# Kernel optimization log

Measured on AMD Instinct MI355X. Metric: run time of the kernel, lower is better.

The kernel has to match this reference:

```python
import jax, jax.numpy as jnp
import numpy as np

N = 50000   # nodes
E = 640000  # edges
IN_C, HID_C, OUT_C = 128, 128, 64


def _glorot(key, shape):
    lim = float(np.sqrt(6.0 / (shape[0] + shape[1])))
    return jax.random.uniform(key, shape, jnp.float32, -lim, lim)


def setup_inputs() -> dict:
    key = jax.random.key(0)
    ks = jax.random.split(key, 6)
    x = jax.random.normal(ks[0], (N, IN_C), jnp.float32)
    edge_index = jax.random.randint(ks[1], (2, E), 0, N, dtype=jnp.int64)
    W1 = _glorot(ks[2], (IN_C, HID_C));  b1 = jnp.zeros((HID_C,), jnp.float32)
    W2 = _glorot(ks[3], (HID_C, HID_C)); b2 = jnp.zeros((HID_C,), jnp.float32)
    W3 = _glorot(ks[4], (HID_C, OUT_C)); b3 = jnp.zeros((OUT_C,), jnp.float32)
    return {"x": x, "edge_index": edge_index,
            "W1": W1, "b1": b1, "W2": W2, "b2": b2, "W3": W3, "b3": b3}


def gcn_conv(x, W, b, src, dst, n_nodes):
    """PyG GCNConv (eval): add self-loops, D^-1/2 (A+I) D^-1/2, linear, bias."""
    h = x @ W  # [N, out]
    ones = jnp.ones(src.shape[0], h.dtype)
    # degree including the self-loop (+1 per node)
    deg = jax.ops.segment_sum(ones, dst, num_segments=n_nodes) + 1.0
    dinv_sqrt = jax.lax.rsqrt(deg)
    coef = dinv_sqrt[src] * dinv_sqrt[dst]               # [E]
    agg = jax.ops.segment_sum(h[src] * coef[:, None], dst, num_segments=n_nodes)
    agg = agg + h * (1.0 / deg)[:, None]                 # self-loop term: 1/deg[i]
    return agg + b


def reference(x, edge_index, W1, b1, W2, b2, W3, b3):
    src, dst = edge_index[0], edge_index[1]
    h = jax.nn.relu(gcn_conv(x, W1, b1, src, dst, N))
    h = jax.nn.relu(gcn_conv(h, W2, b2, src, dst, N))
    return gcn_conv(h, W3, b3, src, dst, N)
```

## Files before the change

kernel.cpp:

```cpp
#include <hip/hip_runtime.h>


#define K_DIM 128

typedef __attribute__((ext_vector_type(8))) short bf16x8;
typedef __attribute__((ext_vector_type(4))) float f32x4;

__device__ __forceinline__ unsigned short f2bf(float x) {
    unsigned u = __float_as_uint(x);
    return (unsigned short)((u + 0x7fffu + ((u >> 16) & 1u)) >> 16);
}
__device__ __forceinline__ float bflo(unsigned v) { return __uint_as_float(v << 16); }
__device__ __forceinline__ float bfhi(unsigned v) { return __uint_as_float(v & 0xffff0000u); }


__global__ void k_zero_int(int* __restrict__ p, int n) {
    int i = blockIdx.x * 256 + threadIdx.x;
    if (i < n) p[i] = 0;
}

__global__ void k_count(const int* __restrict__ dst, int* __restrict__ cnt, int E) {
    int e = blockIdx.x * 256 + threadIdx.x;
    if (e < E) atomicAdd(&cnt[dst[e]], 1);
}

__global__ void k_scan_block(const int* __restrict__ cnt, int* __restrict__ rowptr,
                             int* __restrict__ bsum, float* __restrict__ rsd, int n) {
    __shared__ int s[256];
    int t = threadIdx.x;
    int i = blockIdx.x * 256 + t;
    int x = (i < n) ? cnt[i] : 0;
    if (i < n) rsd[i] = rsqrtf((float)x + 1.0f);
    s[t] = x;
    __syncthreads();
#pragma unroll
    for (int d = 1; d < 256; d <<= 1) {
        int v = (t >= d) ? s[t - d] : 0;
        __syncthreads();
        s[t] += v;
        __syncthreads();
    }
    if (i < n) rowptr[i] = s[t] - x;
    if (t == 255) bsum[blockIdx.x] = s[255];
}

__global__ void k_scan_bsums(int* __restrict__ bsum, int nb) {
    __shared__ int s[256];
    int t = threadIdx.x;
    int x = (t < nb) ? bsum[t] : 0;
    s[t] = x;
    __syncthreads();
#pragma unroll
    for (int d = 1; d < 256; d <<= 1) {
        int v = (t >= d) ? s[t - d] : 0;
        __syncthreads();
        s[t] += v;
        __syncthreads();
    }
    if (t < nb) bsum[t] = s[t] - x;
}

__global__ void k_scan_add(int* __restrict__ rowptr, int* __restrict__ cursor,
                           const int* __restrict__ bsum, int n, int E) {
    int i = blockIdx.x * 256 + threadIdx.x;
    if (i < n) {
        int v = rowptr[i] + bsum[i >> 8];
        rowptr[i] = v;
        cursor[i] = v;
    }
    if (i == 0) rowptr[n] = E;
}

__global__ void k_fill(const int* __restrict__ src, const int* __restrict__ dst,
                       int* __restrict__ cursor, int* __restrict__ col, int E) {
    int e = blockIdx.x * 256 + threadIdx.x;
    if (e < E) {
        int d = dst[e];
        int pos = atomicAdd(&cursor[d], 1);
        col[pos] = src[e];
    }
}

__global__ void k_cvt(const float* __restrict__ x, unsigned short* __restrict__ Xb,
                      const float* __restrict__ W1, const float* __restrict__ W2,
                      const float* __restrict__ W3,
                      unsigned short* __restrict__ Wt1, unsigned short* __restrict__ Wt2,
                      unsigned short* __restrict__ Wt3, int nx4) {
    int i = blockIdx.x * 256 + threadIdx.x;
    if (i < nx4) {
        float4 v = *(const float4*)&x[(size_t)i * 4];
        ushort4 o;
        o.x = f2bf(v.x); o.y = f2bf(v.y); o.z = f2bf(v.z); o.w = f2bf(v.w);
        *(ushort4*)&Xb[(size_t)i * 4] = o;
        return;
    }
    int j = i - nx4;
    if (j < 16384) { int n = j >> 7, k = j & 127; Wt1[n * 128 + k] = f2bf(W1[k * 128 + n]); return; }
    j -= 16384;
    if (j < 16384) { int n = j >> 7, k = j & 127; Wt2[n * 128 + k] = f2bf(W2[k * 128 + n]); return; }
    j -= 16384;
    if (j < 8192)  { int n = j >> 7, k = j & 127; Wt3[n * 128 + k] = f2bf(W3[k * 64 + n]); return; }
}

template <int COUT>
__launch_bounds__(256)
__global__ void k_gemm_mfma(const unsigned short* __restrict__ A,
                            const unsigned short* __restrict__ Wt,
                            const float* __restrict__ rsd,
                            unsigned short* __restrict__ Hb, int nrows) {
    constexpr int NT = COUT / 16;
    const int wave = threadIdx.x >> 6;
    const int lane = threadIdx.x & 63;
    const int m16 = lane & 15;
    const int kg  = lane >> 4;
    const int r0w = blockIdx.x * 64 + wave * 16;

    int arow = r0w + m16;
    if (arow >= nrows) arow = nrows - 1;

    bf16x8 a[4];
#pragma unroll
    for (int kb = 0; kb < 4; ++kb)
        a[kb] = *(const bf16x8*)&A[(size_t)arow * 128 + kb * 32 + kg * 8];

    f32x4 acc[NT];
#pragma unroll
    for (int t = 0; t < NT; ++t) acc[t] = (f32x4){0.f, 0.f, 0.f, 0.f};

#pragma unroll
    for (int t = 0; t < NT; ++t) {
        const unsigned short* wp = &Wt[(size_t)(t * 16 + m16) * 128 + kg * 8];
#pragma unroll
        for (int kb = 0; kb < 4; ++kb) {
            bf16x8 b = *(const bf16x8*)&wp[kb * 32];
            acc[t] = __builtin_amdgcn_mfma_f32_16x16x32_bf16(a[kb], b, acc[t], 0, 0, 0);
        }
    }

    const int rowb = r0w + kg * 4;
    float rs[4];
#pragma unroll
    for (int i = 0; i < 4; ++i)
        rs[i] = (rowb + i < nrows) ? rsd[rowb + i] : 0.0f;

#pragma unroll
    for (int t = 0; t < NT; ++t) {
#pragma unroll
        for (int i = 0; i < 4; ++i) {
            int r = rowb + i;
            if (r < nrows)
                Hb[(size_t)r * COUT + t * 16 + m16] = f2bf(acc[t][i] * rs[i]);
        }
    }
}

template <int C>
__launch_bounds__(256)
__global__ void k_agg_bf(const unsigned short* __restrict__ Hb,
                         const int* __restrict__ rowptr, const int* __restrict__ col,
                         const float* __restrict__ rsd, const float* __restrict__ bias,
                         unsigned short* __restrict__ Ab, int n) {
    constexpr int TPN = C / 8;
    constexpr int NPB = 256 / TPN;
    const int node = blockIdx.x * NPB + threadIdx.x / TPN;
    const int c = (threadIdx.x % TPN) * 8;
    if (node >= n) return;

    float acc[8];
    {
        uint4 v = *(const uint4*)&Hb[(size_t)node * C + c];
        acc[0] = bflo(v.x); acc[1] = bfhi(v.x);
        acc[2] = bflo(v.y); acc[3] = bfhi(v.y);
        acc[4] = bflo(v.z); acc[5] = bfhi(v.z);
        acc[6] = bflo(v.w); acc[7] = bfhi(v.w);
    }
    int e = rowptr[node], end = rowptr[node + 1];
    for (; e + 1 < end; e += 2) {
        int s0 = col[e], s1 = col[e + 1];
        uint4 v0 = *(const uint4*)&Hb[(size_t)s0 * C + c];
        uint4 v1 = *(const uint4*)&Hb[(size_t)s1 * C + c];
        acc[0] += bflo(v0.x); acc[1] += bfhi(v0.x);
        acc[2] += bflo(v0.y); acc[3] += bfhi(v0.y);
        acc[4] += bflo(v0.z); acc[5] += bfhi(v0.z);
        acc[6] += bflo(v0.w); acc[7] += bfhi(v0.w);
        acc[0] += bflo(v1.x); acc[1] += bfhi(v1.x);
        acc[2] += bflo(v1.y); acc[3] += bfhi(v1.y);
        acc[4] += bflo(v1.z); acc[5] += bfhi(v1.z);
        acc[6] += bflo(v1.w); acc[7] += bfhi(v1.w);
    }
    if (e < end) {
        int s0 = col[e];
        uint4 v0 = *(const uint4*)&Hb[(size_t)s0 * C + c];
        acc[0] += bflo(v0.x); acc[1] += bfhi(v0.x);
        acc[2] += bflo(v0.y); acc[3] += bfhi(v0.y);
        acc[4] += bflo(v0.z); acc[5] += bfhi(v0.z);
        acc[6] += bflo(v0.w); acc[7] += bfhi(v0.w);
    }

    const float rs = rsd[node];
    const float4 b0 = *(const float4*)&bias[c];
    const float4 b1 = *(const float4*)&bias[c + 4];
    float r[8];
    r[0] = fmaxf(b0.x + rs * acc[0], 0.0f); r[1] = fmaxf(b0.y + rs * acc[1], 0.0f);
    r[2] = fmaxf(b0.z + rs * acc[2], 0.0f); r[3] = fmaxf(b0.w + rs * acc[3], 0.0f);
    r[4] = fmaxf(b1.x + rs * acc[4], 0.0f); r[5] = fmaxf(b1.y + rs * acc[5], 0.0f);
    r[6] = fmaxf(b1.z + rs * acc[6], 0.0f); r[7] = fmaxf(b1.w + rs * acc[7], 0.0f);

    uint4 o;
    o.x = (unsigned)f2bf(r[0]) | ((unsigned)f2bf(r[1]) << 16);
    o.y = (unsigned)f2bf(r[2]) | ((unsigned)f2bf(r[3]) << 16);
    o.z = (unsigned)f2bf(r[4]) | ((unsigned)f2bf(r[5]) << 16);
    o.w = (unsigned)f2bf(r[6]) | ((unsigned)f2bf(r[7]) << 16);
    *(uint4*)&Ab[(size_t)node * C + c] = o;
}

template <int C>
__launch_bounds__(256)
__global__ void k_agg_final(const unsigned short* __restrict__ Hb,
                            const int* __restrict__ rowptr, const int* __restrict__ col,
                            const float* __restrict__ rsd, const float* __restrict__ bias,
                            float* __restrict__ OUT, int n) {
    constexpr int TPN = C / 8;
    constexpr int NPB = 256 / TPN;
    const int node = blockIdx.x * NPB + threadIdx.x / TPN;
    const int c = (threadIdx.x % TPN) * 8;
    if (node >= n) return;

    float acc[8];
    {
        uint4 v = *(const uint4*)&Hb[(size_t)node * C + c];
        acc[0] = bflo(v.x); acc[1] = bfhi(v.x);
        acc[2] = bflo(v.y); acc[3] = bfhi(v.y);
        acc[4] = bflo(v.z); acc[5] = bfhi(v.z);
        acc[6] = bflo(v.w); acc[7] = bfhi(v.w);
    }
    int e = rowptr[node], end = rowptr[node + 1];
    for (; e + 1 < end; e += 2) {
        int s0 = col[e], s1 = col[e + 1];
        uint4 v0 = *(const uint4*)&Hb[(size_t)s0 * C + c];
        uint4 v1 = *(const uint4*)&Hb[(size_t)s1 * C + c];
        acc[0] += bflo(v0.x); acc[1] += bfhi(v0.x);
        acc[2] += bflo(v0.y); acc[3] += bfhi(v0.y);
        acc[4] += bflo(v0.z); acc[5] += bfhi(v0.z);
        acc[6] += bflo(v0.w); acc[7] += bfhi(v0.w);
        acc[0] += bflo(v1.x); acc[1] += bfhi(v1.x);
        acc[2] += bflo(v1.y); acc[3] += bfhi(v1.y);
        acc[4] += bflo(v1.z); acc[5] += bfhi(v1.z);
        acc[6] += bflo(v1.w); acc[7] += bfhi(v1.w);
    }
    if (e < end) {
        int s0 = col[e];
        uint4 v0 = *(const uint4*)&Hb[(size_t)s0 * C + c];
        acc[0] += bflo(v0.x); acc[1] += bfhi(v0.x);
        acc[2] += bflo(v0.y); acc[3] += bfhi(v0.y);
        acc[4] += bflo(v0.z); acc[5] += bfhi(v0.z);
        acc[6] += bflo(v0.w); acc[7] += bfhi(v0.w);
    }

    const float rs = rsd[node];
    const float4 b0 = *(const float4*)&bias[c];
    const float4 b1 = *(const float4*)&bias[c + 4];
    float* po = &OUT[(size_t)node * C + c];
    *(float4*)&po[0] = make_float4(b0.x + rs * acc[0], b0.y + rs * acc[1],
                                   b0.z + rs * acc[2], b0.w + rs * acc[3]);
    *(float4*)&po[4] = make_float4(b1.x + rs * acc[4], b1.y + rs * acc[5],
                                   b1.z + rs * acc[6], b1.w + rs * acc[7]);
}


extern "C" void kernel_launch(void* const* d_in, const int* in_sizes, int n_in,
                              void* d_out, int out_size, void* d_ws, size_t ws_size,
                              hipStream_t stream) {
    const float* x  = (const float*)d_in[0];
    const int*   ei = (const int*)d_in[1];
    const float* W1 = (const float*)d_in[2];
    const float* b1 = (const float*)d_in[3];
    const float* W2 = (const float*)d_in[4];
    const float* b2 = (const float*)d_in[5];
    const float* W3 = (const float*)d_in[6];
    const float* b3 = (const float*)d_in[7];

    const int N = in_sizes[0] / K_DIM;
    const int E = in_sizes[1] / 2;
    const int* srcv = ei;
    const int* dstv = ei + E;

    char* ws = (char*)d_ws;
    size_t off = 0;
    auto alloc = [&](size_t bytes) {
        char* p = ws + off;
        off += (bytes + 255) & ~(size_t)255;
        return p;
    };
    int*   cnt    = (int*)alloc((size_t)N * 4);
    int*   rowptr = (int*)alloc((size_t)(N + 1) * 4);
    int*   cursor = (int*)alloc((size_t)N * 4);
    int*   bsum   = (int*)alloc(256 * 4);
    float* rsd    = (float*)alloc((size_t)N * 4);
    int*   col    = (int*)alloc((size_t)E * 4);
    unsigned short* Xb  = (unsigned short*)alloc((size_t)N * 128 * 2);
    unsigned short* Wt1 = (unsigned short*)alloc(128 * 128 * 2);
    unsigned short* Wt2 = (unsigned short*)alloc(128 * 128 * 2);
    unsigned short* Wt3 = (unsigned short*)alloc(64 * 128 * 2);
    unsigned short* Hb1 = (unsigned short*)alloc((size_t)N * 128 * 2);
    unsigned short* Ab  = (unsigned short*)alloc((size_t)N * 128 * 2);
    unsigned short* Hb2 = (unsigned short*)alloc((size_t)N * 128 * 2);
    unsigned short* Hb3 = (unsigned short*)alloc((size_t)N * 64 * 2);
    float* out = (float*)d_out;

    const int gN = (N + 255) / 256;
    const int gE = (E + 255) / 256;
    const int gb = (N + 63) / 64;
    const int nb = gN;
    const int gA128 = (N + 15) / 16;
    const int gAF   = (N + 31) / 32;
    const int nx4   = N * 32;
    const int gCVT  = (nx4 + 16384 + 16384 + 8192 + 255) / 256;

    k_zero_int<<<gN, 256, 0, stream>>>(cnt, N);
    k_count<<<gE, 256, 0, stream>>>(dstv, cnt, E);
    k_scan_block<<<nb, 256, 0, stream>>>(cnt, rowptr, bsum, rsd, N);
    k_scan_bsums<<<1, 256, 0, stream>>>(bsum, nb);
    k_scan_add<<<gN, 256, 0, stream>>>(rowptr, cursor, bsum, N, E);
    k_fill<<<gE, 256, 0, stream>>>(srcv, dstv, cursor, col, E);

    k_cvt<<<gCVT, 256, 0, stream>>>(x, Xb, W1, W2, W3, Wt1, Wt2, Wt3, nx4);

    k_gemm_mfma<128><<<gb, 256, 0, stream>>>(Xb, Wt1, rsd, Hb1, N);
    k_agg_bf<128><<<gA128, 256, 0, stream>>>(Hb1, rowptr, col, rsd, b1, Ab, N);

    k_gemm_mfma<128><<<gb, 256, 0, stream>>>(Ab, Wt2, rsd, Hb2, N);
    k_agg_bf<128><<<gA128, 256, 0, stream>>>(Hb2, rowptr, col, rsd, b2, Ab, N);

    k_gemm_mfma<64><<<gb, 256, 0, stream>>>(Ab, Wt3, rsd, Hb3, N);
    k_agg_final<64><<<gAF, 256, 0, stream>>>(Hb3, rowptr, col, rsd, b3, out, N);
}
```

Baseline: 288.5 us.

## Fuse CSR build, input conversion and first GEMM into persistent megakernel

```diff
diff --git a/kernel.cpp b/kernel.cpp
--- a/kernel.cpp
+++ b/kernel.cpp
@@ -13,93 +13,164 @@
 __device__ __forceinline__ float bflo(unsigned v) { return __uint_as_float(v << 16); }
 __device__ __forceinline__ float bfhi(unsigned v) { return __uint_as_float(v & 0xffff0000u); }
 
-
-__global__ void k_zero_int(int* __restrict__ p, int n) {
-    int i = blockIdx.x * 256 + threadIdx.x;
-    if (i < n) p[i] = 0;
-}
-
-__global__ void k_count(const int* __restrict__ dst, int* __restrict__ cnt, int E) {
-    int e = blockIdx.x * 256 + threadIdx.x;
-    if (e < E) atomicAdd(&cnt[dst[e]], 1);
-}
-
-__global__ void k_scan_block(const int* __restrict__ cnt, int* __restrict__ rowptr,
-                             int* __restrict__ bsum, float* __restrict__ rsd, int n) {
+__device__ __forceinline__ void gbar(int* bar, int nb, int ph) {
+    __threadfence();
+    __syncthreads();
+    if (threadIdx.x == 0) {
+        atomicAdd(bar, 1);
+        while (atomicAdd(bar, 0) < nb * ph) __builtin_amdgcn_s_sleep(2);
+    }
+    __syncthreads();
+}
+
+template <int COUT>
+__device__ __forceinline__ void gemm_tile(const unsigned short* __restrict__ A,
+                                          const unsigned short* __restrict__ Wt,
+                                          const float* __restrict__ rsd,
+                                          unsigned short* __restrict__ Hb,
+                                          int nrows, int tile, int tid) {
+    constexpr int NT = COUT / 16;
+    const int wave = tid >> 6;
+    const int lane = tid & 63;
+    const int m16 = lane & 15;
+    const int kg  = lane >> 4;
+    const int r0w = tile * 64 + wave * 16;
+
+    int arow = r0w + m16;
+    if (arow >= nrows) arow = nrows - 1;
+
+    bf16x8 a[4];
+#pragma unroll
+    for (int kb = 0; kb < 4; ++kb)
+        a[kb] = *(const bf16x8*)&A[(size_t)arow * 128 + kb * 32 + kg * 8];
+
+    f32x4 acc[NT];
+#pragma unroll
+    for (int t = 0; t < NT; ++t) acc[t] = (f32x4){0.f, 0.f, 0.f, 0.f};
+
+#pragma unroll
+    for (int t = 0; t < NT; ++t) {
+        const unsigned short* wp = &Wt[(size_t)(t * 16 + m16) * 128 + kg * 8];
+#pragma unroll
+        for (int kb = 0; kb < 4; ++kb) {
+            bf16x8 b = *(const bf16x8*)&wp[kb * 32];
+            acc[t] = __builtin_amdgcn_mfma_f32_16x16x32_bf16(a[kb], b, acc[t], 0, 0, 0);
+        }
+    }
+
+    const int rowb = r0w + kg * 4;
+    float rs[4];
+#pragma unroll
+    for (int i = 0; i < 4; ++i)
+        rs[i] = (rowb + i < nrows) ? rsd[rowb + i] : 0.0f;
+
+#pragma unroll
+    for (int t = 0; t < NT; ++t) {
+#pragma unroll
+        for (int i = 0; i < 4; ++i) {
+            int r = rowb + i;
+            if (r < nrows)
+                Hb[(size_t)r * COUT + t * 16 + m16] = f2bf(acc[t][i] * rs[i]);
+        }
+    }
+}
+
+__global__ void k_init(int* __restrict__ cnt, int* __restrict__ bar,
+                       const float* __restrict__ W1, const float* __restrict__ W2,
+                       const float* __restrict__ W3,
+                       unsigned short* __restrict__ Wt1, unsigned short* __restrict__ Wt2,
+                       unsigned short* __restrict__ Wt3, int n) {
+    int g = blockIdx.x * 256 + threadIdx.x;
+    if (g < n) cnt[g] = 0;
+    if (g == 0) *bar = 0;
+    int j = g;
+    if (j < 16384) { int nn = j >> 7, k = j & 127; Wt1[nn * 128 + k] = f2bf(W1[k * 128 + nn]); return; }
+    j -= 16384;
+    if (j < 16384) { int nn = j >> 7, k = j & 127; Wt2[nn * 128 + k] = f2bf(W2[k * 128 + nn]); return; }
+    j -= 16384;
+    if (j < 8192)  { int nn = j >> 7, k = j & 127; Wt3[nn * 128 + k] = f2bf(W3[k * 64 + nn]); return; }
+}
+
+__global__ __launch_bounds__(256, 2)
+void k_mega(const float* __restrict__ x, const int* __restrict__ src,
+            const int* __restrict__ dst, int* __restrict__ cnt,
+            int* __restrict__ rowptr, int* __restrict__ cursor,
+            int* __restrict__ bsum, int* __restrict__ bsc,
+            float* __restrict__ rsd, int* __restrict__ col,
+            unsigned short* __restrict__ Xb, const unsigned short* __restrict__ Wt1,
+            unsigned short* __restrict__ Hb1, int* __restrict__ bar,
+            int N, int E, int nscan) {
+    const int nb = gridDim.x;
+    const int bid = blockIdx.x, tid = threadIdx.x;
+    const int gsz = nb * 256;
+    const int g = bid * 256 + tid;
     __shared__ int s[256];
-    int t = threadIdx.x;
-    int i = blockIdx.x * 256 + t;
-    int x = (i < n) ? cnt[i] : 0;
-    if (i < n) rsd[i] = rsqrtf((float)x + 1.0f);
-    s[t] = x;
-    __syncthreads();
-#pragma unroll
-    for (int d = 1; d < 256; d <<= 1) {
-        int v = (t >= d) ? s[t - d] : 0;
-        __syncthreads();
-        s[t] += v;
-        __syncthreads();
-    }
-    if (i < n) rowptr[i] = s[t] - x;
-    if (t == 255) bsum[blockIdx.x] = s[255];
-}
-
-__global__ void k_scan_bsums(int* __restrict__ bsum, int nb) {
-    __shared__ int s[256];
-    int t = threadIdx.x;
-    int x = (t < nb) ? bsum[t] : 0;
-    s[t] = x;
-    __syncthreads();
-#pragma unroll
-    for (int d = 1; d < 256; d <<= 1) {
-        int v = (t >= d) ? s[t - d] : 0;
-        __syncthreads();
-        s[t] += v;
-        __syncthreads();
-    }
-    if (t < nb) bsum[t] = s[t] - x;
-}
-
-__global__ void k_scan_add(int* __restrict__ rowptr, int* __restrict__ cursor,
-                           const int* __restrict__ bsum, int n, int E) {
-    int i = blockIdx.x * 256 + threadIdx.x;
-    if (i < n) {
-        int v = rowptr[i] + bsum[i >> 8];
-        rowptr[i] = v;
-        cursor[i] = v;
-    }
-    if (i == 0) rowptr[n] = E;
-}
-
-__global__ void k_fill(const int* __restrict__ src, const int* __restrict__ dst,
-                       int* __restrict__ cursor, int* __restrict__ col, int E) {
-    int e = blockIdx.x * 256 + threadIdx.x;
-    if (e < E) {
-        int d = dst[e];
-        int pos = atomicAdd(&cursor[d], 1);
-        col[pos] = src[e];
-    }
-}
-
-__global__ void k_cvt(const float* __restrict__ x, unsigned short* __restrict__ Xb,
-                      const float* __restrict__ W1, const float* __restrict__ W2,
-                      const float* __restrict__ W3,
-                      unsigned short* __restrict__ Wt1, unsigned short* __restrict__ Wt2,
-                      unsigned short* __restrict__ Wt3, int nx4) {
-    int i = blockIdx.x * 256 + threadIdx.x;
-    if (i < nx4) {
+
+    for (int e = g; e < E; e += gsz) atomicAdd(&cnt[dst[e]], 1);
+    const int nx4 = N * 32;
+    for (int i = g; i < nx4; i += gsz) {
         float4 v = *(const float4*)&x[(size_t)i * 4];
         ushort4 o;
         o.x = f2bf(v.x); o.y = f2bf(v.y); o.z = f2bf(v.z); o.w = f2bf(v.w);
         *(ushort4*)&Xb[(size_t)i * 4] = o;
-        return;
-    }
-    int j = i - nx4;
-    if (j < 16384) { int n = j >> 7, k = j & 127; Wt1[n * 128 + k] = f2bf(W1[k * 128 + n]); return; }
-    j -= 16384;
-    if (j < 16384) { int n = j >> 7, k = j & 127; Wt2[n * 128 + k] = f2bf(W2[k * 128 + n]); return; }
-    j -= 16384;
-    if (j < 8192)  { int n = j >> 7, k = j & 127; Wt3[n * 128 + k] = f2bf(W3[k * 64 + n]); return; }
+    }
+    gbar(bar, nb, 1);
+
+    if (bid < nscan) {
+        int i = bid * 256 + tid;
+        int v = (i < N) ? cnt[i] : 0;
+        if (i < N) rsd[i] = rsqrtf((float)v + 1.0f);
+        s[tid] = v;
+        __syncthreads();
+#pragma unroll
+        for (int d = 1; d < 256; d <<= 1) {
+            int u = (tid >= d) ? s[tid - d] : 0;
+            __syncthreads();
+            s[tid] += u;
+            __syncthreads();
+        }
+        if (i < N) rowptr[i] = s[tid] - v;
+        if (tid == 255) atomicExch(&bsum[bid], s[255]);
+    }
+    gbar(bar, nb, 2);
+
+    if (bid == 0) {
+        int v = (tid < nscan) ? atomicAdd(&bsum[tid], 0) : 0;
+        s[tid] = v;
+        __syncthreads();
+#pragma unroll
+        for (int d = 1; d < 256; d <<= 1) {
+            int u = (tid >= d) ? s[tid - d] : 0;
+            __syncthreads();
+            s[tid] += u;
+            __syncthreads();
+        }
+        if (tid < nscan) bsc[tid] = s[tid] - v;
+    }
+    gbar(bar, nb, 3);
+
+    if (bid < nscan) {
+        int off0 = bsc[bid];
+        int i = bid * 256 + tid;
+        if (i < N) {
+            int v = rowptr[i] + off0;
+            rowptr[i] = v;
+            cursor[i] = v;
+        }
+    }
+    if (g == 0) rowptr[N] = E;
+    gbar(bar, nb, 4);
+
+    for (int e = g; e < E; e += gsz) {
+        int d = dst[e];
+        int pos = atomicAdd(&cursor[d], 1);
+        col[pos] = src[e];
+    }
+    gbar(bar, nb, 5);
+
+    const int ntiles = (N + 63) >> 6;
+    for (int t = bid; t < ntiles; t += nb)
+        gemm_tile<128>(Xb, Wt1, rsd, Hb1, N, t, tid);
 }
 
 template <int COUT>
@@ -108,50 +179,7 @@
                             const unsigned short* __restrict__ Wt,
                             const float* __restrict__ rsd,
                             unsigned short* __restrict__ Hb, int nrows) {
-    constexpr int NT = COUT / 16;
-    const int wave = threadIdx.x >> 6;
-    const int lane = threadIdx.x & 63;
-    const int m16 = lane & 15;
-    const int kg  = lane >> 4;
-    const int r0w = blockIdx.x * 64 + wave * 16;
-
-    int arow = r0w + m16;
-    if (arow >= nrows) arow = nrows - 1;
-
-    bf16x8 a[4];
-#pragma unroll
-    for (int kb = 0; kb < 4; ++kb)
-        a[kb] = *(const bf16x8*)&A[(size_t)arow * 128 + kb * 32 + kg * 8];
-
-    f32x4 acc[NT];
-#pragma unroll
-    for (int t = 0; t < NT; ++t) acc[t] = (f32x4){0.f, 0.f, 0.f, 0.f};
-
-#pragma unroll
-    for (int t = 0; t < NT; ++t) {
-        const unsigned short* wp = &Wt[(size_t)(t * 16 + m16) * 128 + kg * 8];
-#pragma unroll
-        for (int kb = 0; kb < 4; ++kb) {
-            bf16x8 b = *(const bf16x8*)&wp[kb * 32];
-            acc[t] = __builtin_amdgcn_mfma_f32_16x16x32_bf16(a[kb], b, acc[t], 0, 0, 0);
-        }
-    }
-
-    const int rowb = r0w + kg * 4;
-    float rs[4];
-#pragma unroll
-    for (int i = 0; i < 4; ++i)
-        rs[i] = (rowb + i < nrows) ? rsd[rowb + i] : 0.0f;
-
-#pragma unroll
-    for (int t = 0; t < NT; ++t) {
-#pragma unroll
-        for (int i = 0; i < 4; ++i) {
-            int r = rowb + i;
-            if (r < nrows)
-                Hb[(size_t)r * COUT + t * 16 + m16] = f2bf(acc[t][i] * rs[i]);
-        }
-    }
+    gemm_tile<COUT>(A, Wt, rsd, Hb, nrows, blockIdx.x, threadIdx.x);
 }
 
 template <int C>
@@ -175,10 +203,12 @@
         acc[6] = bflo(v.w); acc[7] = bfhi(v.w);
     }
     int e = rowptr[node], end = rowptr[node + 1];
-    for (; e + 1 < end; e += 2) {
-        int s0 = col[e], s1 = col[e + 1];
+    for (; e + 3 < end; e += 4) {
+        int s0 = col[e], s1 = col[e + 1], s2 = col[e + 2], s3 = col[e + 3];
         uint4 v0 = *(const uint4*)&Hb[(size_t)s0 * C + c];
         uint4 v1 = *(const uint4*)&Hb[(size_t)s1 * C + c];
+        uint4 v2 = *(const uint4*)&Hb[(size_t)s2 * C + c];
+        uint4 v3 = *(const uint4*)&Hb[(size_t)s3 * C + c];
         acc[0] += bflo(v0.x); acc[1] += bfhi(v0.x);
         acc[2] += bflo(v0.y); acc[3] += bfhi(v0.y);
         acc[4] += bflo(v0.z); acc[5] += bfhi(v0.z);
@@ -187,8 +217,16 @@
         acc[2] += bflo(v1.y); acc[3] += bfhi(v1.y);
         acc[4] += bflo(v1.z); acc[5] += bfhi(v1.z);
         acc[6] += bflo(v1.w); acc[7] += bfhi(v1.w);
-    }
-    if (e < end) {
+        acc[0] += bflo(v2.x); acc[1] += bfhi(v2.x);
+        acc[2] += bflo(v2.y); acc[3] += bfhi(v2.y);
+        acc[4] += bflo(v2.z); acc[5] += bfhi(v2.z);
+        acc[6] += bflo(v2.w); acc[7] += bfhi(v2.w);
+        acc[0] += bflo(v3.x); acc[1] += bfhi(v3.x);
+        acc[2] += bflo(v3.y); acc[3] += bfhi(v3.y);
+        acc[4] += bflo(v3.z); acc[5] += bfhi(v3.z);
+        acc[6] += bflo(v3.w); acc[7] += bfhi(v3.w);
+    }
+    for (; e < end; ++e) {
         int s0 = col[e];
         uint4 v0 = *(const uint4*)&Hb[(size_t)s0 * C + c];
         acc[0] += bflo(v0.x); acc[1] += bfhi(v0.x);
@@ -235,10 +273,12 @@
         acc[6] = bflo(v.w); acc[7] = bfhi(v.w);
     }
     int e = rowptr[node], end = rowptr[node + 1];
-    for (; e + 1 < end; e += 2) {
-        int s0 = col[e], s1 = col[e + 1];
+    for (; e + 3 < end; e += 4) {
+        int s0 = col[e], s1 = col[e + 1], s2 = col[e + 2], s3 = col[e + 3];
         uint4 v0 = *(const uint4*)&Hb[(size_t)s0 * C + c];
         uint4 v1 = *(const uint4*)&Hb[(size_t)s1 * C + c];
+        uint4 v2 = *(const uint4*)&Hb[(size_t)s2 * C + c];
+        uint4 v3 = *(const uint4*)&Hb[(size_t)s3 * C + c];
         acc[0] += bflo(v0.x); acc[1] += bfhi(v0.x);
         acc[2] += bflo(v0.y); acc[3] += bfhi(v0.y);
         acc[4] += bflo(v0.z); acc[5] += bfhi(v0.z);
@@ -247,8 +287,16 @@
         acc[2] += bflo(v1.y); acc[3] += bfhi(v1.y);
         acc[4] += bflo(v1.z); acc[5] += bfhi(v1.z);
         acc[6] += bflo(v1.w); acc[7] += bfhi(v1.w);
-    }
-    if (e < end) {
+        acc[0] += bflo(v2.x); acc[1] += bfhi(v2.x);
+        acc[2] += bflo(v2.y); acc[3] += bfhi(v2.y);
+        acc[4] += bflo(v2.z); acc[5] += bfhi(v2.z);
+        acc[6] += bflo(v2.w); acc[7] += bfhi(v2.w);
+        acc[0] += bflo(v3.x); acc[1] += bfhi(v3.x);
+        acc[2] += bflo(v3.y); acc[3] += bfhi(v3.y);
+        acc[4] += bflo(v3.z); acc[5] += bfhi(v3.z);
+        acc[6] += bflo(v3.w); acc[7] += bfhi(v3.w);
+    }
+    for (; e < end; ++e) {
         int s0 = col[e];
         uint4 v0 = *(const uint4*)&Hb[(size_t)s0 * C + c];
         acc[0] += bflo(v0.x); acc[1] += bfhi(v0.x);
@@ -296,6 +344,8 @@
     int*   rowptr = (int*)alloc((size_t)(N + 1) * 4);
     int*   cursor = (int*)alloc((size_t)N * 4);
     int*   bsum   = (int*)alloc(256 * 4);
+    int*   bsc    = (int*)alloc(256 * 4);
+    int*   bar    = (int*)alloc(256);
     float* rsd    = (float*)alloc((size_t)N * 4);
     int*   col    = (int*)alloc((size_t)E * 4);
     unsigned short* Xb  = (unsigned short*)alloc((size_t)N * 128 * 2);
@@ -308,30 +358,20 @@
     unsigned short* Hb3 = (unsigned short*)alloc((size_t)N * 64 * 2);
     float* out = (float*)d_out;
 
-    const int gN = (N + 255) / 256;
-    const int gE = (E + 255) / 256;
-    const int gb = (N + 63) / 64;
-    const int nb = gN;
+    const int gN    = (N + 255) / 256;
+    const int gb    = (N + 63) / 64;
     const int gA128 = (N + 15) / 16;
     const int gAF   = (N + 31) / 32;
-    const int nx4   = N * 32;
-    const int gCVT  = (nx4 + 16384 + 16384 + 8192 + 255) / 256;
-
-    k_zero_int<<<gN, 256, 0, stream>>>(cnt, N);
-    k_count<<<gE, 256, 0, stream>>>(dstv, cnt, E);
-    k_scan_block<<<nb, 256, 0, stream>>>(cnt, rowptr, bsum, rsd, N);
-    k_scan_bsums<<<1, 256, 0, stream>>>(bsum, nb);
-    k_scan_add<<<gN, 256, 0, stream>>>(rowptr, cursor, bsum, N, E);
-    k_fill<<<gE, 256, 0, stream>>>(srcv, dstv, cursor, col, E);
-
-    k_cvt<<<gCVT, 256, 0, stream>>>(x, Xb, W1, W2, W3, Wt1, Wt2, Wt3, nx4);
-
-    k_gemm_mfma<128><<<gb, 256, 0, stream>>>(Xb, Wt1, rsd, Hb1, N);
+    const int NB    = 512;
+
+    k_init<<<gN, 256, 0, stream>>>(cnt, bar, W1, W2, W3, Wt1, Wt2, Wt3, N);
+
+    k_mega<<<NB, 256, 0, stream>>>(x, srcv, dstv, cnt, rowptr, cursor, bsum, bsc,
+                                   rsd, col, Xb, Wt1, Hb1, bar, N, E, gN);
+
     k_agg_bf<128><<<gA128, 256, 0, stream>>>(Hb1, rowptr, col, rsd, b1, Ab, N);
-
     k_gemm_mfma<128><<<gb, 256, 0, stream>>>(Ab, Wt2, rsd, Hb2, N);
     k_agg_bf<128><<<gA128, 256, 0, stream>>>(Hb2, rowptr, col, rsd, b2, Ab, N);
-
     k_gemm_mfma<64><<<gb, 256, 0, stream>>>(Ab, Wt3, rsd, Hb3, N);
     k_agg_final<64><<<gAF, 256, 0, stream>>>(Hb3, rowptr, col, rsd, b3, out, N);
 }
```

Result: slower. 589.8 us (+104.4%).

## Fuse aggregation with next-layer GEMM and merge setup kernels to cut launches

Applied to the files above, without the earlier changes.

```diff
diff --git a/kernel.cpp b/kernel.cpp
--- a/kernel.cpp
+++ b/kernel.cpp
@@ -13,15 +13,91 @@
 __device__ __forceinline__ float bflo(unsigned v) { return __uint_as_float(v << 16); }
 __device__ __forceinline__ float bfhi(unsigned v) { return __uint_as_float(v & 0xffff0000u); }
 
-
-__global__ void k_zero_int(int* __restrict__ p, int n) {
+__device__ __forceinline__ void add8(float* acc, uint4 v) {
+    acc[0] += bflo(v.x); acc[1] += bfhi(v.x);
+    acc[2] += bflo(v.y); acc[3] += bfhi(v.y);
+    acc[4] += bflo(v.z); acc[5] += bfhi(v.z);
+    acc[6] += bflo(v.w); acc[7] += bfhi(v.w);
+}
+
+template <int COUT>
+__device__ __forceinline__ void gemm_tile(const unsigned short* __restrict__ A,
+                                          const unsigned short* __restrict__ Wt,
+                                          const float* __restrict__ rsd,
+                                          unsigned short* __restrict__ Hb,
+                                          int nrows, int tile, int tid) {
+    constexpr int NT = COUT / 16;
+    const int wave = tid >> 6;
+    const int lane = tid & 63;
+    const int m16 = lane & 15;
+    const int kg  = lane >> 4;
+    const int r0w = tile * 64 + wave * 16;
+
+    int arow = r0w + m16;
+    if (arow >= nrows) arow = nrows - 1;
+
+    bf16x8 a[4];
+#pragma unroll
+    for (int kb = 0; kb < 4; ++kb)
+        a[kb] = *(const bf16x8*)&A[(size_t)arow * 128 + kb * 32 + kg * 8];
+
+    f32x4 acc[NT];
+#pragma unroll
+    for (int t = 0; t < NT; ++t) acc[t] = (f32x4){0.f, 0.f, 0.f, 0.f};
+
+#pragma unroll
+    for (int t = 0; t < NT; ++t) {
+        const unsigned short* wp = &Wt[(size_t)(t * 16 + m16) * 128 + kg * 8];
+#pragma unroll
+        for (int kb = 0; kb < 4; ++kb) {
+            bf16x8 b = *(const bf16x8*)&wp[kb * 32];
+            acc[t] = __builtin_amdgcn_mfma_f32_16x16x32_bf16(a[kb], b, acc[t], 0, 0, 0);
+        }
+    }
+
+    const int rowb = r0w + kg * 4;
+#pragma unroll
+    for (int t = 0; t < NT; ++t) {
+#pragma unroll
+        for (int i = 0; i < 4; ++i) {
+            int r = rowb + i;
+            if (r < nrows)
+                Hb[(size_t)r * COUT + t * 16 + m16] = f2bf(acc[t][i] * rsd[r]);
+        }
+    }
+}
+
+__global__ void k_init(int* __restrict__ cnt, int n) {
     int i = blockIdx.x * 256 + threadIdx.x;
-    if (i < n) p[i] = 0;
-}
-
-__global__ void k_count(const int* __restrict__ dst, int* __restrict__ cnt, int E) {
-    int e = blockIdx.x * 256 + threadIdx.x;
-    if (e < E) atomicAdd(&cnt[dst[e]], 1);
+    if (i < n) cnt[i] = 0;
+}
+
+__global__ void k_count_cvt(const int* __restrict__ dst, int* __restrict__ cnt,
+                            const float* __restrict__ x, unsigned short* __restrict__ Xb,
+                            const float* __restrict__ W1, const float* __restrict__ W2,
+                            const float* __restrict__ W3,
+                            unsigned short* __restrict__ Wt1, unsigned short* __restrict__ Wt2,
+                            unsigned short* __restrict__ Wt3,
+                            int E, int nx4, int gCount) {
+    if ((int)blockIdx.x < gCount) {
+        int e = blockIdx.x * 256 + threadIdx.x;
+        if (e < E) atomicAdd(&cnt[dst[e]], 1);
+        return;
+    }
+    int g = (blockIdx.x - gCount) * 256 + threadIdx.x;
+    if (g < nx4) {
+        float4 v = *(const float4*)&x[(size_t)g * 4];
+        ushort4 o;
+        o.x = f2bf(v.x); o.y = f2bf(v.y); o.z = f2bf(v.z); o.w = f2bf(v.w);
+        *(ushort4*)&Xb[(size_t)g * 4] = o;
+        return;
+    }
+    int j = g - nx4;
+    if (j < 16384) { int nn = j >> 7, k = j & 127; Wt1[nn * 128 + k] = f2bf(W1[k * 128 + nn]); return; }
+    j -= 16384;
+    if (j < 16384) { int nn = j >> 7, k = j & 127; Wt2[nn * 128 + k] = f2bf(W2[k * 128 + nn]); return; }
+    j -= 16384;
+    if (j < 8192)  { int nn = j >> 7, k = j & 127; Wt3[nn * 128 + k] = f2bf(W3[k * 64 + nn]); return; }
 }
 
 __global__ void k_scan_block(const int* __restrict__ cnt, int* __restrict__ rowptr,
@@ -29,189 +105,166 @@
     __shared__ int s[256];
     int t = threadIdx.x;
     int i = blockIdx.x * 256 + t;
-    int x = (i < n) ? cnt[i] : 0;
-    if (i < n) rsd[i] = rsqrtf((float)x + 1.0f);
-    s[t] = x;
+    int v = (i < n) ? cnt[i] : 0;
+    if (i < n) rsd[i] = rsqrtf((float)v + 1.0f);
+    s[t] = v;
     __syncthreads();
 #pragma unroll
     for (int d = 1; d < 256; d <<= 1) {
-        int v = (t >= d) ? s[t - d] : 0;
+        int u = (t >= d) ? s[t - d] : 0;
         __syncthreads();
-        s[t] += v;
+        s[t] += u;
         __syncthreads();
     }
-    if (i < n) rowptr[i] = s[t] - x;
+    if (i < n) rowptr[i] = s[t] - v;
     if (t == 255) bsum[blockIdx.x] = s[255];
 }
 
-__global__ void k_scan_bsums(int* __restrict__ bsum, int nb) {
+__global__ void k_scan_add(const int* __restrict__ bsum, int* __restrict__ rowptr,
+                           int* __restrict__ cursor, int n, int E, int nscan) {
     __shared__ int s[256];
+    __shared__ int off;
     int t = threadIdx.x;
-    int x = (t < nb) ? bsum[t] : 0;
-    s[t] = x;
+    int v = (t < nscan) ? bsum[t] : 0;
+    s[t] = v;
     __syncthreads();
 #pragma unroll
     for (int d = 1; d < 256; d <<= 1) {
-        int v = (t >= d) ? s[t - d] : 0;
+        int u = (t >= d) ? s[t - d] : 0;
         __syncthreads();
-        s[t] += v;
+        s[t] += u;
         __syncthreads();
     }
-    if (t < nb) bsum[t] = s[t] - x;
-}
-
-__global__ void k_scan_add(int* __restrict__ rowptr, int* __restrict__ cursor,
-                           const int* __restrict__ bsum, int n, int E) {
-    int i = blockIdx.x * 256 + threadIdx.x;
+    if (t == (int)blockIdx.x) off = s[t] - v;
+    __syncthreads();
+    int i = blockIdx.x * 256 + t;
     if (i < n) {
-        int v = rowptr[i] + bsum[i >> 8];
-        rowptr[i] = v;
-        cursor[i] = v;
+        int val = rowptr[i] + off;
+        rowptr[i] = val;
+        cursor[i] = val;
     }
     if (i == 0) rowptr[n] = E;
 }
 
-__global__ void k_fill(const int* __restrict__ src, const int* __restrict__ dst,
-                       int* __restrict__ cursor, int* __restrict__ col, int E) {
-    int e = blockIdx.x * 256 + threadIdx.x;
-    if (e < E) {
-        int d = dst[e];
-        int pos = atomicAdd(&cursor[d], 1);
-        col[pos] = src[e];
-    }
-}
-
-__global__ void k_cvt(const float* __restrict__ x, unsigned short* __restrict__ Xb,
-                      const float* __restrict__ W1, const float* __restrict__ W2,
-                      const float* __restrict__ W3,
-                      unsigned short* __restrict__ Wt1, unsigned short* __restrict__ Wt2,
-                      unsigned short* __restrict__ Wt3, int nx4) {
-    int i = blockIdx.x * 256 + threadIdx.x;
-    if (i < nx4) {
-        float4 v = *(const float4*)&x[(size_t)i * 4];
-        ushort4 o;
-        o.x = f2bf(v.x); o.y = f2bf(v.y); o.z = f2bf(v.z); o.w = f2bf(v.w);
-        *(ushort4*)&Xb[(size_t)i * 4] = o;
+__global__ __launch_bounds__(256)
+void k_fill_gemm1(const int* __restrict__ src, const int* __restrict__ dst,
+                  int* __restrict__ cursor, int* __restrict__ col,
+                  const unsigned short* __restrict__ Xb, const unsigned short* __restrict__ Wt1,
+                  const float* __restrict__ rsd, unsigned short* __restrict__ Hb1,
+                  int N, int E, int gFill) {
+    if ((int)blockIdx.x < gFill) {
+        int e = blockIdx.x * 256 + threadIdx.x;
+        if (e < E) {
+            int d = dst[e];
+            int pos = atomicAdd(&cursor[d], 1);
+            col[pos] = src[e];
+        }
         return;
     }
-    int j = i - nx4;
-    if (j < 16384) { int n = j >> 7, k = j & 127; Wt1[n * 128 + k] = f2bf(W1[k * 128 + n]); return; }
-    j -= 16384;
-    if (j < 16384) { int n = j >> 7, k = j & 127; Wt2[n * 128 + k] = f2bf(W2[k * 128 + n]); return; }
-    j -= 16384;
-    if (j < 8192)  { int n = j >> 7, k = j & 127; Wt3[n * 128 + k] = f2bf(W3[k * 64 + n]); return; }
+    gemm_tile<128>(Xb, Wt1, rsd, Hb1, N, blockIdx.x - gFill, threadIdx.x);
 }
 
 template <int COUT>
 __launch_bounds__(256)
-__global__ void k_gemm_mfma(const unsigned short* __restrict__ A,
-                            const unsigned short* __restrict__ Wt,
-                            const float* __restrict__ rsd,
-                            unsigned short* __restrict__ Hb, int nrows) {
-    constexpr int NT = COUT / 16;
-    const int wave = threadIdx.x >> 6;
-    const int lane = threadIdx.x & 63;
+__global__ void k_agg_gemm(const unsigned short* __restrict__ Hin,
+                           const int* __restrict__ rowptr, const int* __restrict__ col,
+                           const float* __restrict__ rsd, const float* __restrict__ bias,
+                           const unsigned short* __restrict__ Wt,
+                           unsigned short* __restrict__ Hout, int n) {
+    constexpr int NT = COUT / 32;
+    __shared__ unsigned short As[32][136];
+    const int tid = threadIdx.x;
+    const int r0 = blockIdx.x * 32;
+
+    {
+        const int lr = tid >> 3;
+        const int lc = (tid & 7) * 16;
+        const int row = r0 + lr;
+        const int rc = (row < n) ? row : (n - 1);
+
+        float acc[16];
+#pragma unroll
+        for (int j = 0; j < 16; ++j) acc[j] = 0.0f;
+        {
+            const unsigned short* hp = &Hin[(size_t)rc * 128 + lc];
+            add8(acc, *(const uint4*)hp);
+            add8(acc + 8, *(const uint4*)(hp + 8));
+        }
+        int e = rowptr[rc], end = rowptr[rc + 1];
+        for (; e + 1 < end; e += 2) {
+            const unsigned short* p0 = &Hin[(size_t)col[e] * 128 + lc];
+            const unsigned short* p1 = &Hin[(size_t)col[e + 1] * 128 + lc];
+            uint4 a0 = *(const uint4*)p0, a1 = *(const uint4*)(p0 + 8);
+            uint4 c0 = *(const uint4*)p1, c1 = *(const uint4*)(p1 + 8);
+            add8(acc, a0); add8(acc + 8, a1);
+            add8(acc, c0); add8(acc + 8, c1);
+        }
+        if (e < end) {
+            const unsigned short* p0 = &Hin[(size_t)col[e] * 128 + lc];
+            add8(acc, *(const uint4*)p0);
+            add8(acc + 8, *(const uint4*)(p0 + 8));
+        }
+
+        const float rs = rsd[rc];
+        float r[16];
+#pragma unroll
+        for (int q = 0; q < 4; ++q) {
+            float4 bq = *(const float4*)&bias[lc + q * 4];
+            r[q * 4 + 0] = fmaxf(bq.x + rs * acc[q * 4 + 0], 0.0f);
+            r[q * 4 + 1] = fmaxf(bq.y + rs * acc[q * 4 + 1], 0.0f);
+            r[q * 4 + 2] = fmaxf(bq.z + rs * acc[q * 4 + 2], 0.0f);
+            r[q * 4 + 3] = fmaxf(bq.w + rs * acc[q * 4 + 3], 0.0f);
+        }
+        uint4 o0, o1;
+        o0.x = (unsigned)f2bf(r[0])  | ((unsigned)f2bf(r[1])  << 16);
+        o0.y = (unsigned)f2bf(r[2])  | ((unsigned)f2bf(r[3])  << 16);
+        o0.z = (unsigned)f2bf(r[4])  | ((unsigned)f2bf(r[5])  << 16);
+        o0.w = (unsigned)f2bf(r[6])  | ((unsigned)f2bf(r[7])  << 16);
+        o1.x = (unsigned)f2bf(r[8])  | ((unsigned)f2bf(r[9])  << 16);
+        o1.y = (unsigned)f2bf(r[10]) | ((unsigned)f2bf(r[11]) << 16);
+        o1.z = (unsigned)f2bf(r[12]) | ((unsigned)f2bf(r[13]) << 16);
+        o1.w = (unsigned)f2bf(r[14]) | ((unsigned)f2bf(r[15]) << 16);
+        *(uint4*)&As[lr][lc] = o0;
+        *(uint4*)&As[lr][lc + 8] = o1;
+    }
+    __syncthreads();
+
+    const int wave = tid >> 6;
+    const int lane = tid & 63;
     const int m16 = lane & 15;
     const int kg  = lane >> 4;
-    const int r0w = blockIdx.x * 64 + wave * 16;
-
-    int arow = r0w + m16;
-    if (arow >= nrows) arow = nrows - 1;
+    const int rloc = (wave >> 1) * 16 + m16;
+    const int cbase = (wave & 1) * (COUT / 2);
 
     bf16x8 a[4];
 #pragma unroll
     for (int kb = 0; kb < 4; ++kb)
-        a[kb] = *(const bf16x8*)&A[(size_t)arow * 128 + kb * 32 + kg * 8];
-
-    f32x4 acc[NT];
-#pragma unroll
-    for (int t = 0; t < NT; ++t) acc[t] = (f32x4){0.f, 0.f, 0.f, 0.f};
+        a[kb] = *(const bf16x8*)&As[rloc][kb * 32 + kg * 8];
+
+    f32x4 acc2[NT];
+#pragma unroll
+    for (int t = 0; t < NT; ++t) acc2[t] = (f32x4){0.f, 0.f, 0.f, 0.f};
 
 #pragma unroll
     for (int t = 0; t < NT; ++t) {
-        const unsigned short* wp = &Wt[(size_t)(t * 16 + m16) * 128 + kg * 8];
+        const unsigned short* wp = &Wt[(size_t)(cbase + t * 16 + m16) * 128 + kg * 8];
 #pragma unroll
         for (int kb = 0; kb < 4; ++kb) {
             bf16x8 b = *(const bf16x8*)&wp[kb * 32];
-            acc[t] = __builtin_amdgcn_mfma_f32_16x16x32_bf16(a[kb], b, acc[t], 0, 0, 0);
-        }
-    }
-
-    const int rowb = r0w + kg * 4;
-    float rs[4];
-#pragma unroll
-    for (int i = 0; i < 4; ++i)
-        rs[i] = (rowb + i < nrows) ? rsd[rowb + i] : 0.0f;
-
+            acc2[t] = __builtin_amdgcn_mfma_f32_16x16x32_bf16(a[kb], b, acc2[t], 0, 0, 0);
+        }
+    }
+
+    const int rowb = r0 + (wave >> 1) * 16 + kg * 4;
 #pragma unroll
     for (int t = 0; t < NT; ++t) {
 #pragma unroll
         for (int i = 0; i < 4; ++i) {
             int r = rowb + i;
-            if (r < nrows)
-                Hb[(size_t)r * COUT + t * 16 + m16] = f2bf(acc[t][i] * rs[i]);
-        }
-    }
-}
-
-template <int C>
-__launch_bounds__(256)
-__global__ void k_agg_bf(const unsigned short* __restrict__ Hb,
-                         const int* __restrict__ rowptr, const int* __restrict__ col,
-                         const float* __restrict__ rsd, const float* __restrict__ bias,
-                         unsigned short* __restrict__ Ab, int n) {
-    constexpr int TPN = C / 8;
-    constexpr int NPB = 256 / TPN;
-    const int node = blockIdx.x * NPB + threadIdx.x / TPN;
-    const int c = (threadIdx.x % TPN) * 8;
-    if (node >= n) return;
-
-    float acc[8];
-    {
-        uint4 v = *(const uint4*)&Hb[(size_t)node * C + c];
-        acc[0] = bflo(v.x); acc[1] = bfhi(v.x);
-        acc[2] = bflo(v.y); acc[3] = bfhi(v.y);
-        acc[4] = bflo(v.z); acc[5] = bfhi(v.z);
-        acc[6] = bflo(v.w); acc[7] = bfhi(v.w);
-    }
-    int e = rowptr[node], end = rowptr[node + 1];
-    for (; e + 1 < end; e += 2) {
-        int s0 = col[e], s1 = col[e + 1];
-        uint4 v0 = *(const uint4*)&Hb[(size_t)s0 * C + c];
-        uint4 v1 = *(const uint4*)&Hb[(size_t)s1 * C + c];
-        acc[0] += bflo(v0.x); acc[1] += bfhi(v0.x);
-        acc[2] += bflo(v0.y); acc[3] += bfhi(v0.y);
-        acc[4] += bflo(v0.z); acc[5] += bfhi(v0.z);
-        acc[6] += bflo(v0.w); acc[7] += bfhi(v0.w);
-        acc[0] += bflo(v1.x); acc[1] += bfhi(v1.x);
-        acc[2] += bflo(v1.y); acc[3] += bfhi(v1.y);
-        acc[4] += bflo(v1.z); acc[5] += bfhi(v1.z);
-        acc[6] += bflo(v1.w); acc[7] += bfhi(v1.w);
-    }
-    if (e < end) {
-        int s0 = col[e];
-        uint4 v0 = *(const uint4*)&Hb[(size_t)s0 * C + c];
-        acc[0] += bflo(v0.x); acc[1] += bfhi(v0.x);
-        acc[2] += bflo(v0.y); acc[3] += bfhi(v0.y);
-        acc[4] += bflo(v0.z); acc[5] += bfhi(v0.z);
-        acc[6] += bflo(v0.w); acc[7] += bfhi(v0.w);
-    }
-
-    const float rs = rsd[node];
-    const float4 b0 = *(const float4*)&bias[c];
-    const float4 b1 = *(const float4*)&bias[c + 4];
-    float r[8];
-    r[0] = fmaxf(b0.x + rs * acc[0], 0.0f); r[1] = fmaxf(b0.y + rs * acc[1], 0.0f);
-    r[2] = fmaxf(b0.z + rs * acc[2], 0.0f); r[3] = fmaxf(b0.w + rs * acc[3], 0.0f);
-    r[4] = fmaxf(b1.x + rs * acc[4], 0.0f); r[5] = fmaxf(b1.y + rs * acc[5], 0.0f);
-    r[6] = fmaxf(b1.z + rs * acc[6], 0.0f); r[7] = fmaxf(b1.w + rs * acc[7], 0.0f);
-
-    uint4 o;
-    o.x = (unsigned)f2bf(r[0]) | ((unsigned)f2bf(r[1]) << 16);
-    o.y = (unsigned)f2bf(r[2]) | ((unsigned)f2bf(r[3]) << 16);
-    o.z = (unsigned)f2bf(r[4]) | ((unsigned)f2bf(r[5]) << 16);
-    o.w = (unsigned)f2bf(r[6]) | ((unsigned)f2bf(r[7]) << 16);
-    *(uint4*)&Ab[(size_t)node * C + c] = o;
+            if (r < n)
+                Hout[(size_t)r * COUT + cbase + t * 16 + m16] = f2bf(acc2[t][i] * rsd[r]);
+        }
+    }
 }
 
 template <int C>
@@ -227,35 +280,20 @@
     if (node >= n) return;
 
     float acc[8];
-    {
-        uint4 v = *(const uint4*)&Hb[(size_t)node * C + c];
-        acc[0] = bflo(v.x); acc[1] = bfhi(v.x);
-        acc[2] = bflo(v.y); acc[3] = bfhi(v.y);
-        acc[4] = bflo(v.z); acc[5] = bfhi(v.z);
-        acc[6] = bflo(v.w); acc[7] = bfhi(v.w);
-    }
+#pragma unroll
+    for (int j = 0; j < 8; ++j) acc[j] = 0.0f;
+    add8(acc, *(const uint4*)&Hb[(size_t)node * C + c]);
+
     int e = rowptr[node], end = rowptr[node + 1];
-    for (; e + 1 < end; e += 2) {
-        int s0 = col[e], s1 = col[e + 1];
-        uint4 v0 = *(const uint4*)&Hb[(size_t)s0 * C + c];
-        uint4 v1 = *(const uint4*)&Hb[(size_t)s1 * C + c];
-        acc[0] += bflo(v0.x); acc[1] += bfhi(v0.x);
-        acc[2] += bflo(v0.y); acc[3] += bfhi(v0.y);
-        acc[4] += bflo(v0.z); acc[5] += bfhi(v0.z);
-        acc[6] += bflo(v0.w); acc[7] += bfhi(v0.w);
-        acc[0] += bflo(v1.x); acc[1] += bfhi(v1.x);
-        acc[2] += bflo(v1.y); acc[3] += bfhi(v1.y);
-        acc[4] += bflo(v1.z); acc[5] += bfhi(v1.z);
-        acc[6] += bflo(v1.w); acc[7] += bfhi(v1.w);
-    }
-    if (e < end) {
-        int s0 = col[e];
-        uint4 v0 = *(const uint4*)&Hb[(size_t)s0 * C + c];
-        acc[0] += bflo(v0.x); acc[1] += bfhi(v0.x);
-        acc[2] += bflo(v0.y); acc[3] += bfhi(v0.y);
-        acc[4] += bflo(v0.z); acc[5] += bfhi(v0.z);
-        acc[6] += bflo(v0.w); acc[7] += bfhi(v0.w);
-    }
+    for (; e + 3 < end; e += 4) {
+        uint4 v0 = *(const uint4*)&Hb[(size_t)col[e]     * C + c];
+        uint4 v1 = *(const uint4*)&Hb[(size_t)col[e + 1] * C + c];
+        uint4 v2 = *(const uint4*)&Hb[(size_t)col[e + 2] * C + c];
+        uint4 v3 = *(const uint4*)&Hb[(size_t)col[e + 3] * C + c];
+        add8(acc, v0); add8(acc, v1); add8(acc, v2); add8(acc, v3);
+    }
+    for (; e < end; ++e)
+        add8(acc, *(const uint4*)&Hb[(size_t)col[e] * C + c]);
 
     const float rs = rsd[node];
     const float4 b0 = *(const float4*)&bias[c];
@@ -303,35 +341,27 @@
     unsigned short* Wt2 = (unsigned short*)alloc(128 * 128 * 2);
     unsigned short* Wt3 = (unsigned short*)alloc(64 * 128 * 2);
     unsigned short* Hb1 = (unsigned short*)alloc((size_t)N * 128 * 2);
-    unsigned short* Ab  = (unsigned short*)alloc((size_t)N * 128 * 2);
     unsigned short* Hb2 = (unsigned short*)alloc((size_t)N * 128 * 2);
     unsigned short* Hb3 = (unsigned short*)alloc((size_t)N * 64 * 2);
     float* out = (float*)d_out;
 
-    const int gN = (N + 255) / 256;
-    const int gE = (E + 255) / 256;
-    const int gb = (N + 63) / 64;
-    const int nb = gN;
-    const int gA128 = (N + 15) / 16;
-    const int gAF   = (N + 31) / 32;
-    const int nx4   = N * 32;
-    const int gCVT  = (nx4 + 16384 + 16384 + 8192 + 255) / 256;
-
-    k_zero_int<<<gN, 256, 0, stream>>>(cnt, N);
-    k_count<<<gE, 256, 0, stream>>>(dstv, cnt, E);
-    k_scan_block<<<nb, 256, 0, stream>>>(cnt, rowptr, bsum, rsd, N);
-    k_scan_bsums<<<1, 256, 0, stream>>>(bsum, nb);
-    k_scan_add<<<gN, 256, 0, stream>>>(rowptr, cursor, bsum, N, E);
-    k_fill<<<gE, 256, 0, stream>>>(srcv, dstv, cursor, col, E);
-
-    k_cvt<<<gCVT, 256, 0, stream>>>(x, Xb, W1, W2, W3, Wt1, Wt2, Wt3, nx4);
-
-    k_gemm_mfma<128><<<gb, 256, 0, stream>>>(Xb, Wt1, rsd, Hb1, N);
-    k_agg_bf<128><<<gA128, 256, 0, stream>>>(Hb1, rowptr, col, rsd, b1, Ab, N);
-
-    k_gemm_mfma<128><<<gb, 256, 0, stream>>>(Ab, Wt2, rsd, Hb2, N);
-    k_agg_bf<128><<<gA128, 256, 0, stream>>>(Hb2, rowptr, col, rsd, b2, Ab, N);
-
-    k_gemm_mfma<64><<<gb, 256, 0, stream>>>(Ab, Wt3, rsd, Hb3, N);
-    k_agg_final<64><<<gAF, 256, 0, stream>>>(Hb3, rowptr, col, rsd, b3, out, N);
-}
+    const int gN     = (N + 255) / 256;
+    const int gCount = (E + 255) / 256;
+    const int nx4    = N * 32;
+    const int gX     = (nx4 + 255) / 256;
+    const int gW     = (16384 + 16384 + 8192 + 255) / 256;
+    const int gTiles = (N + 63) / 64;
+    const int gF     = (N + 31) / 32;
+
+    k_init<<<gN, 256, 0, stream>>>(cnt, N);
+    k_count_cvt<<<gCount + gX + gW, 256, 0, stream>>>(dstv, cnt, x, Xb, W1, W2, W3,
+                                                      Wt1, Wt2, Wt3, E, nx4, gCount);
+    k_scan_block<<<gN, 256, 0, stream>>>(cnt, rowptr, bsum, rsd, N);
+    k_scan_add<<<gN, 256, 0, stream>>>(bsum, rowptr, cursor, N, E, gN);
+    k_fill_gemm1<<<gCount + gTiles, 256, 0, stream>>>(srcv, dstv, cursor, col,
+                                                      Xb, Wt1, rsd, Hb1, N, E, gCount);
+
+    k_agg_gemm<128><<<gF, 256, 0, stream>>>(Hb1, rowptr, col, rsd, b1, Wt2, Hb2, N);
+    k_agg_gemm<64><<<gF, 256, 0, stream>>>(Hb2, rowptr, col, rsd, b2, Wt3, Hb3, N);
+    k_agg_final<64><<<gF, 256, 0, stream>>>(Hb3, rowptr, col, rsd, b3, out, N);
+}
```

Result: faster. 269.1 us (-6.7%).
